# Optimization experiments

Measured on AMD Instinct MI355X. Metric: run time of the kernel, lower is better.

## Reference

```python
import jax, jax.numpy as jnp
import numpy as np
from jax import lax

ALPHA = 100.0          # SuperSpike surrogate slope (method='super', alpha=100)
DT_TAU_MEM = 0.1       # dt * tau_mem_inv = 0.001 * 100
DT_TAU_SYN = 0.2       # dt * tau_syn_inv = 0.001 * 200
V_TH = 1.0
SEQ = 40

@jax.custom_vjp
def spike(x):
    return (x > 0).astype(x.dtype)

def _spike_fwd(x):
    return (x > 0).astype(x.dtype), x

def _spike_bwd(x, g):
    # SuperSpike surrogate gradient: 1 / (alpha*|x| + 1)^2
    return (g / (ALPHA * jnp.abs(x) + 1.0) ** 2,)

spike.defvjp(_spike_fwd, _spike_bwd)

def encode(current):
    # ConstantCurrentLIFEncoder: LIF driven by constant current, SEQ steps.
    def step(v, _):
        v = v + DT_TAU_MEM * (-v + current)   # v_leak = 0
        z = spike(v - V_TH)
        v = v * (1.0 - z)                     # v_reset = 0
        return v, z
    _, zs = lax.scan(step, jnp.zeros_like(current), None, length=SEQ)
    return zs  # (SEQ, B, F)

def setup_inputs() -> dict:
    key = jax.random.key(0)
    ks = jax.random.split(key, 5)
    B = 16384
    x = jax.random.normal(ks[0], (B, 4), jnp.float32)
    w_in = jax.random.normal(ks[1], (128, 8), jnp.float32) * np.sqrt(2.0 / 8)
    w_rec = jax.random.normal(ks[2], (128, 128), jnp.float32) * np.sqrt(2.0 / 128)
    w_out = jax.random.normal(ks[3], (2, 128), jnp.float32) * np.sqrt(2.0 / 128)
    keep = jax.random.bernoulli(ks[4], 0.5, (SEQ, B, 128))
    dropout_mask = keep.astype(jnp.float32) * 2.0  # inverted dropout, p=0.5
    return {"x": x, "w_in": w_in, "w_rec": w_rec, "w_out": w_out,
            "dropout_mask": dropout_mask}

def reference(x, w_in, w_rec, w_out, dropout_mask):
    scale = 50.0
    x_pos = encode(jax.nn.relu(scale * x))     # (T, B, 4)
    x_neg = encode(jax.nn.relu(-scale * x))    # (T, B, 4)
    xs = jnp.concatenate([x_pos, x_neg], axis=2)  # (T, B, 8)

    B = x.shape[0]
    H = w_rec.shape[0]
    O = w_out.shape[0]
    z0 = jnp.zeros((B, H), x.dtype)
    v0 = jnp.zeros((B, H), x.dtype)
    i0 = jnp.zeros((B, H), x.dtype)
    vo0 = jnp.zeros((B, O), x.dtype)
    io0 = jnp.zeros((B, O), x.dtype)

    def step(carry, inp):
        z, v, i, vo, io = carry
        xt, mt = inp
        # LIFCell (recurrent)
        v_dec = v + DT_TAU_MEM * (-v + i)
        i_dec = i * (1.0 - DT_TAU_SYN)
        z_new = spike(v_dec - V_TH)
        v_new = (1.0 - z_new) * v_dec
        i_new = i_dec + xt @ w_in.T + z @ w_rec.T
        # Dropout on spikes
        z_d = z_new * mt
        # LICell readout
        vo_new = vo + DT_TAU_MEM * (-vo + io)
        io_new = io * (1.0 - DT_TAU_SYN) + z_d @ w_out.T
        return (z_new, v_new, i_new, vo_new, io_new), vo_new

    _, voltages = lax.scan(step, (z0, v0, i0, vo0, io0), (xs, dropout_mask))
    m = jnp.max(voltages, axis=0)          # (B, O)
    return jax.nn.softmax(m, axis=1)
```

## Files before the change

kernel.cpp:

```cpp
#include <hip/hip_runtime.h>
#include <cstdint>

#define T_SEQ 40
#define NB    16384
#define NH    128
#define NROWS 136
#define ROWD  129
#define WPB   16
#define NTHR  (WPB * 64)
#define NBLK  512

typedef float v2f __attribute__((ext_vector_type(2)));

template <int C>
__device__ __forceinline__ float dppstep(float v) {
  int t = __builtin_amdgcn_update_dpp(0, __float_as_int(v), C, 0xF, 0xF, true);
  return v + __int_as_float(t);
}
__device__ __forceinline__ void wave_sum2(float &a, float &b) {
  a = dppstep<0x111>(a); b = dppstep<0x111>(b);
  a = dppstep<0x112>(a); b = dppstep<0x112>(b);
  a = dppstep<0x114>(a); b = dppstep<0x114>(b);
  a = dppstep<0x118>(a); b = dppstep<0x118>(b);
  a = dppstep<0x142>(a); b = dppstep<0x142>(b);
  a = dppstep<0x143>(a); b = dppstep<0x143>(b);
  a = __int_as_float(__builtin_amdgcn_readlane(__float_as_int(a), 63));
  b = __int_as_float(__builtin_amdgcn_readlane(__float_as_int(b), 63));
}

__global__ __launch_bounds__(NTHR, 8)
void Policy_22033182228693_kernel(const float* __restrict__ x,
                                  const float* __restrict__ w_in,
                                  const float* __restrict__ w_rec,
                                  const float* __restrict__ w_out,
                                  const float* __restrict__ dmask,
                                  float* __restrict__ out)
{
  __shared__ float W[NROWS * ROWD];

  const int tid = threadIdx.x;
  for (int e = tid; e < NH * NH; e += NTHR) {
    int h = e >> 7, j = e & 127;
    W[j * ROWD + h] = w_rec[e];
  }
  for (int e = tid; e < NH * 8; e += NTHR) {
    int h = e >> 3, k = e & 7;
    W[(128 + k) * ROWD + h] = w_in[e];
  }
  __syncthreads();

  const int wave = tid >> 6;
  const int lane = tid & 63;
  const int gw   = blockIdx.x * WPB + wave;

  const float wo00 = w_out[lane];
  const float wo01 = w_out[lane + 64];
  const float wo10 = w_out[128 + lane];
  const float wo11 = w_out[192 + lane];

  const size_t TS = (size_t)NB * NH;

#pragma unroll 1
  for (int rr = 0; rr < 2; ++rr) {
    const int b = gw * 2 + rr;

    float xv = x[(size_t)b * 4 + (lane & 3)];
    float cc = fmaxf(0.f, ((lane & 4) ? -50.f : 50.f) * xv);
    if (lane >= 8) cc = 0.f;

    bool always = cc > 10.f;
    uint64_t aM = __ballot((int)always);
    if (always) cc = 0.f;
    v2f cin; cin.x = 0.f; cin.y = 0.f;
    for (uint64_t m = aM; m; m &= m - 1) {
      int o = (128 + __builtin_ctzll(m)) * ROWD;
      cin.x += W[o + lane];
      cin.y += W[o + lane + 64];
    }

    const float* gmu = dmask + (size_t)b * NH;
    float mc0 = gmu[lane],      mc1 = gmu[lane + 64];
    float mn0 = gmu[TS + lane], mn1 = gmu[TS + lane + 64];

    float ve = 0.f;
    v2f v;  v.x = 0.f;  v.y = 0.f;
    v2f i;  i.x = 0.f;  i.y = 0.f;
    float io0 = 0.f, io1 = 0.f, vo0 = 0.f, vo1 = 0.f;
    float m0 = -3.0e38f, m1 = -3.0e38f;
    uint64_t bE = 0, bO = 0;

#pragma unroll 1
    for (int t = 0; t < T_SEQ; ++t) {
      ve += 0.1f * (cc - ve);
      bool zi = ve > 1.0f;
      if (zi) ve = 0.f;
      uint64_t bI = __ballot((int)zi);

      v2f vd = v + 0.1f * (i - v);
      bool z0 = vd.x > 1.0f, z1 = vd.y > 1.0f;
      v.x = z0 ? 0.f : vd.x;
      v.y = z1 ? 0.f : vd.y;

      v2f a = 0.8f * i;
      {
        uint64_t mA = bE, mB = bO;
        int nA = __popcll(mA), nB = __popcll(mB);
        int nP = nA < nB ? nA : nB;
        if (nP > 0) {
          int oA = __builtin_ctzll(mA) * ROWD;        mA &= mA - 1;
          int oB = (64 + __builtin_ctzll(mB)) * ROWD; mB &= mB - 1;
          v2f p; p.x = W[oA + lane]; p.y = W[oA + lane + 64];
          v2f q; q.x = W[oB + lane]; q.y = W[oB + lane + 64];
#pragma unroll 2
          for (int k = 1; k < nP; ++k) {
            int o2 = __builtin_ctzll(mA) * ROWD;        mA &= mA - 1;
            int o3 = (64 + __builtin_ctzll(mB)) * ROWD; mB &= mB - 1;
            v2f r; r.x = W[o2 + lane]; r.y = W[o2 + lane + 64];
            v2f s; s.x = W[o3 + lane]; s.y = W[o3 + lane + 64];
            a += p + q;
            p = r; q = s;
          }
          a += p + q;
        }
        uint64_t mR; int rb;
        if (mA) { mR = mA; rb = 0; } else { mR = mB; rb = 64; }
        while (mR) {
          int o = (rb + __builtin_ctzll(mR)) * ROWD; mR &= mR - 1;
          v2f w; w.x = W[o + lane]; w.y = W[o + lane + 64];
          a += w;
        }
        while (bI) {
          int o = (128 + __builtin_ctzll(bI)) * ROWD; bI &= bI - 1;
          v2f w; w.x = W[o + lane]; w.y = W[o + lane + 64];
          a += w;
        }
        a += cin;
      }
      i = a;

      bE = __ballot((int)z0);
      bO = __ballot((int)z1);

      float mt0 = mc0, mt1 = mc1;
      mc0 = mn0; mc1 = mn1;
      int tp = (t + 2 < T_SEQ) ? t + 2 : T_SEQ - 1;
      size_t so = (size_t)tp * TS;
      mn0 = gmu[so + lane];
      mn1 = gmu[so + lane + 64];

      float zd0 = z0 ? mt0 : 0.f;
      float zd1 = z1 ? mt1 : 0.f;
      float u0 = zd0 * wo00 + zd1 * wo01;
      float u1 = zd0 * wo10 + zd1 * wo11;
      if (bE | bO) {
        wave_sum2(u0, u1);
      } else {
        u0 = 0.f; u1 = 0.f;
      }

      vo0 += 0.1f * (io0 - vo0);
      vo1 += 0.1f * (io1 - vo1);
      io0 = 0.8f * io0 + u0;
      io1 = 0.8f * io1 + u1;
      m0 = fmaxf(m0, vo0);
      m1 = fmaxf(m1, vo1);
    }

    if (lane == 0) {
      float mx = fmaxf(m0, m1);
      float e0 = expf(m0 - mx), e1 = expf(m1 - mx);
      float inv = 1.f / (e0 + e1);
      ((float2*)out)[b] = make_float2(e0 * inv, e1 * inv);
    }
  }
}

extern "C" void kernel_launch(void* const* d_in, const int* in_sizes, int n_in,
                              void* d_out, int out_size, void* d_ws, size_t ws_size,
                              hipStream_t stream) {
  const float* x     = (const float*)d_in[0];
  const float* w_in  = (const float*)d_in[1];
  const float* w_rec = (const float*)d_in[2];
  const float* w_out = (const float*)d_in[3];
  const float* dmask = (const float*)d_in[4];
  float* out = (float*)d_out;

  hipLaunchKernelGGL(Policy_22033182228693_kernel, dim3(NBLK), dim3(NTHR), 0, stream,
                     x, w_in, w_rec, w_out, dmask, out);
}
```

Baseline: 506.5 us.

## Process two batch rows per wave concurrently with half-wave split and vec4 LDS loads

Instead of each wave running the two batch rows one after the other, each half-wave (32 lanes) now owns one batch row, with four hidden units per lane. The recurrent weights are stored in LDS with a permuted column order and a row stride of 132 so each lane can fetch its four weights with a single 128-bit load. The sparse spike-driven accumulation loops run while any lane still has work, so the loop count follows the busier half of the wave. This halves the serial time steps per wave and cuts the number of LDS instructions, at the cost of divergence between the two rows' spike counts and more registers per lane.

```diff
diff --git a/kernel.cpp b/kernel.cpp
--- a/kernel.cpp
+++ b/kernel.cpp
@@ -5,27 +5,27 @@
 #define NB    16384
 #define NH    128
 #define NROWS 136
-#define ROWD  129
+#define ROWD  132
 #define WPB   16
 #define NTHR  (WPB * 64)
 #define NBLK  512
 
-typedef float v2f __attribute__((ext_vector_type(2)));
+typedef float v4f __attribute__((ext_vector_type(4)));
 
 template <int C>
 __device__ __forceinline__ float dppstep(float v) {
   int t = __builtin_amdgcn_update_dpp(0, __float_as_int(v), C, 0xF, 0xF, true);
   return v + __int_as_float(t);
 }
-__device__ __forceinline__ void wave_sum2(float &a, float &b) {
+__device__ __forceinline__ void half_sum2(float &a, float &b) {
   a = dppstep<0x111>(a); b = dppstep<0x111>(b);
   a = dppstep<0x112>(a); b = dppstep<0x112>(b);
   a = dppstep<0x114>(a); b = dppstep<0x114>(b);
   a = dppstep<0x118>(a); b = dppstep<0x118>(b);
   a = dppstep<0x142>(a); b = dppstep<0x142>(b);
-  a = dppstep<0x143>(a); b = dppstep<0x143>(b);
-  a = __int_as_float(__builtin_amdgcn_readlane(__float_as_int(a), 63));
-  b = __int_as_float(__builtin_amdgcn_readlane(__float_as_int(b), 63));
+}
+__device__ __forceinline__ float rl(float v, int l) {
+  return __int_as_float(__builtin_amdgcn_readlane(__float_as_int(v), l));
 }
 
 __global__ __launch_bounds__(NTHR, 8)
@@ -40,138 +40,147 @@
 
   const int tid = threadIdx.x;
   for (int e = tid; e < NH * NH; e += NTHR) {
-    int h = e >> 7, j = e & 127;
-    W[j * ROWD + h] = w_rec[e];
+    int s = e >> 7, j = e & 127;
+    int h = (s >> 2) + ((s & 3) << 5);
+    W[j * ROWD + s] = w_rec[h * NH + j];
   }
   for (int e = tid; e < NH * 8; e += NTHR) {
-    int h = e >> 3, k = e & 7;
-    W[(128 + k) * ROWD + h] = w_in[e];
+    int s = e >> 3, k = e & 7;
+    int h = (s >> 2) + ((s & 3) << 5);
+    W[(NH + k) * ROWD + s] = w_in[h * 8 + k];
   }
   __syncthreads();
 
   const int wave = tid >> 6;
   const int lane = tid & 63;
+  const int half = lane >> 5;
+  const int c    = lane & 31;
   const int gw   = blockIdx.x * WPB + wave;
+  const int myb  = gw * 2 + half;
+  const float* __restrict__ Wc = W + 4 * c;
 
-  const float wo00 = w_out[lane];
-  const float wo01 = w_out[lane + 64];
-  const float wo10 = w_out[128 + lane];
-  const float wo11 = w_out[192 + lane];
+  const float wo00 = w_out[c],        wo01 = w_out[c + 32];
+  const float wo02 = w_out[c + 64],   wo03 = w_out[c + 96];
+  const float wo10 = w_out[128 + c],  wo11 = w_out[160 + c];
+  const float wo12 = w_out[192 + c],  wo13 = w_out[224 + c];
 
+  float xv = x[(size_t)myb * 4 + (c & 3)];
+  float cc = fmaxf(0.f, ((c & 4) ? -50.f : 50.f) * xv);
+  if (c >= 8) cc = 0.f;
+
+  bool always = cc > 10.f;
+  uint64_t aM = __ballot((int)always);
+  if (always) cc = 0.f;
+  v4f cin = {0.f, 0.f, 0.f, 0.f};
+  {
+    uint32_t mh = (uint32_t)((half ? (aM >> 32) : aM) & 0xffu);
+    while (mh) {
+      int k = __builtin_ctz(mh); mh &= mh - 1;
+      cin += *(const v4f*)&Wc[(NH + k) * ROWD];
+    }
+  }
+
+  const float* gmu = dmask + (size_t)myb * NH;
   const size_t TS = (size_t)NB * NH;
+  float mc0 = gmu[c],      mc1 = gmu[c + 32],      mc2 = gmu[c + 64],      mc3 = gmu[c + 96];
+  float mn0 = gmu[TS + c], mn1 = gmu[TS + c + 32], mn2 = gmu[TS + c + 64], mn3 = gmu[TS + c + 96];
+
+  float ve = 0.f;
+  v4f v = {0.f, 0.f, 0.f, 0.f};
+  v4f i = {0.f, 0.f, 0.f, 0.f};
+  float ioA0 = 0.f, ioA1 = 0.f, voA0 = 0.f, voA1 = 0.f;
+  float ioB0 = 0.f, ioB1 = 0.f, voB0 = 0.f, voB1 = 0.f;
+  float mA0 = -3.0e38f, mA1 = -3.0e38f, mB0 = -3.0e38f, mB1 = -3.0e38f;
+  uint64_t pb0 = 0, pb1 = 0, pb2 = 0, pb3 = 0;
 
 #pragma unroll 1
-  for (int rr = 0; rr < 2; ++rr) {
-    const int b = gw * 2 + rr;
+  for (int t = 0; t < T_SEQ; ++t) {
+    ve += 0.1f * (cc - ve);
+    bool zi = ve > 1.0f;
+    if (zi) ve = 0.f;
+    uint64_t bI = __ballot((int)zi);
 
-    float xv = x[(size_t)b * 4 + (lane & 3)];
-    float cc = fmaxf(0.f, ((lane & 4) ? -50.f : 50.f) * xv);
-    if (lane >= 8) cc = 0.f;
+    v4f vd = v + 0.1f * (i - v);
+    bool z0 = vd.x > 1.0f, z1 = vd.y > 1.0f, z2 = vd.z > 1.0f, z3 = vd.w > 1.0f;
+    v.x = z0 ? 0.f : vd.x;
+    v.y = z1 ? 0.f : vd.y;
+    v.z = z2 ? 0.f : vd.z;
+    v.w = z3 ? 0.f : vd.w;
 
-    bool always = cc > 10.f;
-    uint64_t aM = __ballot((int)always);
-    if (always) cc = 0.f;
-    v2f cin; cin.x = 0.f; cin.y = 0.f;
-    for (uint64_t m = aM; m; m &= m - 1) {
-      int o = (128 + __builtin_ctzll(m)) * ROWD;
-      cin.x += W[o + lane];
-      cin.y += W[o + lane + 64];
+    v4f a = 0.8f * i;
+    {
+      uint32_t q0 = (uint32_t)(half ? (pb0 >> 32) : pb0);
+      uint32_t q1 = (uint32_t)(half ? (pb1 >> 32) : pb1);
+      uint32_t q2 = (uint32_t)(half ? (pb2 >> 32) : pb2);
+      uint32_t q3 = (uint32_t)(half ? (pb3 >> 32) : pb3);
+      uint64_t m01 = (uint64_t)q0 | ((uint64_t)q1 << 32);
+      uint64_t m23 = (uint64_t)q2 | ((uint64_t)q3 << 32);
+      uint32_t mI  = (uint32_t)((half ? (bI >> 32) : bI) & 0xffu);
+
+      while (__any(m01 != 0)) {
+        if (m01) {
+          int j = __builtin_ctzll(m01); m01 &= m01 - 1;
+          a += *(const v4f*)&Wc[j * ROWD];
+        }
+      }
+      while (__any(m23 != 0)) {
+        if (m23) {
+          int j = __builtin_ctzll(m23); m23 &= m23 - 1;
+          a += *(const v4f*)&Wc[(64 + j) * ROWD];
+        }
+      }
+      while (__any(mI != 0)) {
+        if (mI) {
+          int k = __builtin_ctz(mI); mI &= mI - 1;
+          a += *(const v4f*)&Wc[(NH + k) * ROWD];
+        }
+      }
+      a += cin;
+    }
+    i = a;
+
+    pb0 = __ballot((int)z0);
+    pb1 = __ballot((int)z1);
+    pb2 = __ballot((int)z2);
+    pb3 = __ballot((int)z3);
+
+    float mt0 = mc0, mt1 = mc1, mt2 = mc2, mt3 = mc3;
+    mc0 = mn0; mc1 = mn1; mc2 = mn2; mc3 = mn3;
+    int tp = (t + 2 < T_SEQ) ? t + 2 : T_SEQ - 1;
+    size_t so = (size_t)tp * TS;
+    mn0 = gmu[so + c];      mn1 = gmu[so + c + 32];
+    mn2 = gmu[so + c + 64]; mn3 = gmu[so + c + 96];
+
+    float zd0 = z0 ? mt0 : 0.f, zd1 = z1 ? mt1 : 0.f;
+    float zd2 = z2 ? mt2 : 0.f, zd3 = z3 ? mt3 : 0.f;
+    float u0 = zd0 * wo00 + zd1 * wo01 + zd2 * wo02 + zd3 * wo03;
+    float u1 = zd0 * wo10 + zd1 * wo11 + zd2 * wo12 + zd3 * wo13;
+
+    float sA0, sA1, sB0, sB1;
+    if (pb0 | pb1 | pb2 | pb3) {
+      half_sum2(u0, u1);
+      sA0 = rl(u0, 31); sA1 = rl(u1, 31);
+      sB0 = rl(u0, 63); sB1 = rl(u1, 63);
+    } else {
+      sA0 = sA1 = sB0 = sB1 = 0.f;
     }
 
-    const float* gmu = dmask + (size_t)b * NH;
-    float mc0 = gmu[lane],      mc1 = gmu[lane + 64];
-    float mn0 = gmu[TS + lane], mn1 = gmu[TS + lane + 64];
+    voA0 += 0.1f * (ioA0 - voA0);  voA1 += 0.1f * (ioA1 - voA1);
+    voB0 += 0.1f * (ioB0 - voB0);  voB1 += 0.1f * (ioB1 - voB1);
+    ioA0 = 0.8f * ioA0 + sA0;      ioA1 = 0.8f * ioA1 + sA1;
+    ioB0 = 0.8f * ioB0 + sB0;      ioB1 = 0.8f * ioB1 + sB1;
+    mA0 = fmaxf(mA0, voA0);  mA1 = fmaxf(mA1, voA1);
+    mB0 = fmaxf(mB0, voB0);  mB1 = fmaxf(mB1, voB1);
+  }
 
-    float ve = 0.f;
-    v2f v;  v.x = 0.f;  v.y = 0.f;
-    v2f i;  i.x = 0.f;  i.y = 0.f;
-    float io0 = 0.f, io1 = 0.f, vo0 = 0.f, vo1 = 0.f;
-    float m0 = -3.0e38f, m1 = -3.0e38f;
-    uint64_t bE = 0, bO = 0;
-
-#pragma unroll 1
-    for (int t = 0; t < T_SEQ; ++t) {
-      ve += 0.1f * (cc - ve);
-      bool zi = ve > 1.0f;
-      if (zi) ve = 0.f;
-      uint64_t bI = __ballot((int)zi);
-
-      v2f vd = v + 0.1f * (i - v);
-      bool z0 = vd.x > 1.0f, z1 = vd.y > 1.0f;
-      v.x = z0 ? 0.f : vd.x;
-      v.y = z1 ? 0.f : vd.y;
-
-      v2f a = 0.8f * i;
-      {
-        uint64_t mA = bE, mB = bO;
-        int nA = __popcll(mA), nB = __popcll(mB);
-        int nP = nA < nB ? nA : nB;
-        if (nP > 0) {
-          int oA = __builtin_ctzll(mA) * ROWD;        mA &= mA - 1;
-          int oB = (64 + __builtin_ctzll(mB)) * ROWD; mB &= mB - 1;
-          v2f p; p.x = W[oA + lane]; p.y = W[oA + lane + 64];
-          v2f q; q.x = W[oB + lane]; q.y = W[oB + lane + 64];
-#pragma unroll 2
-          for (int k = 1; k < nP; ++k) {
-            int o2 = __builtin_ctzll(mA) * ROWD;        mA &= mA - 1;
-            int o3 = (64 + __builtin_ctzll(mB)) * ROWD; mB &= mB - 1;
-            v2f r; r.x = W[o2 + lane]; r.y = W[o2 + lane + 64];
-            v2f s; s.x = W[o3 + lane]; s.y = W[o3 + lane + 64];
-            a += p + q;
-            p = r; q = s;
-          }
-          a += p + q;
-        }
-        uint64_t mR; int rb;
-        if (mA) { mR = mA; rb = 0; } else { mR = mB; rb = 64; }
-        while (mR) {
-          int o = (rb + __builtin_ctzll(mR)) * ROWD; mR &= mR - 1;
-          v2f w; w.x = W[o + lane]; w.y = W[o + lane + 64];
-          a += w;
-        }
-        while (bI) {
-          int o = (128 + __builtin_ctzll(bI)) * ROWD; bI &= bI - 1;
-          v2f w; w.x = W[o + lane]; w.y = W[o + lane + 64];
-          a += w;
-        }
-        a += cin;
-      }
-      i = a;
-
-      bE = __ballot((int)z0);
-      bO = __ballot((int)z1);
-
-      float mt0 = mc0, mt1 = mc1;
-      mc0 = mn0; mc1 = mn1;
-      int tp = (t + 2 < T_SEQ) ? t + 2 : T_SEQ - 1;
-      size_t so = (size_t)tp * TS;
-      mn0 = gmu[so + lane];
-      mn1 = gmu[so + lane + 64];
-
-      float zd0 = z0 ? mt0 : 0.f;
-      float zd1 = z1 ? mt1 : 0.f;
-      float u0 = zd0 * wo00 + zd1 * wo01;
-      float u1 = zd0 * wo10 + zd1 * wo11;
-      if (bE | bO) {
-        wave_sum2(u0, u1);
-      } else {
-        u0 = 0.f; u1 = 0.f;
-      }
-
-      vo0 += 0.1f * (io0 - vo0);
-      vo1 += 0.1f * (io1 - vo1);
-      io0 = 0.8f * io0 + u0;
-      io1 = 0.8f * io1 + u1;
-      m0 = fmaxf(m0, vo0);
-      m1 = fmaxf(m1, vo1);
-    }
-
-    if (lane == 0) {
-      float mx = fmaxf(m0, m1);
-      float e0 = expf(m0 - mx), e1 = expf(m1 - mx);
-      float inv = 1.f / (e0 + e1);
-      ((float2*)out)[b] = make_float2(e0 * inv, e1 * inv);
-    }
+  if (lane == 0) {
+    float mxA = fmaxf(mA0, mA1);
+    float eA0 = expf(mA0 - mxA), eA1 = expf(mA1 - mxA);
+    float invA = 1.f / (eA0 + eA1);
+    float mxB = fmaxf(mB0, mB1);
+    float eB0 = expf(mB0 - mxB), eB1 = expf(mB1 - mxB);
+    float invB = 1.f / (eB0 + eB1);
+    ((float4*)out)[gw] = make_float4(eA0 * invA, eA1 * invA, eB0 * invB, eB1 * invB);
   }
 }
 
```

New measurement: 571.0 us. 1.13x slower.
